# Optimization experiments

Hardware: AMD Instinct MI355X
Metric: run time of the kernel (lower is better)

Reference implementation:

```python
import jax, jax.numpy as jnp
import numpy as np

D_MODEL = 1024
NUM_HEADS = 16
D_K = D_MODEL // NUM_HEADS
THETA = 10000.0
SEQ = 4096
BATCH = 1


def _rope(x, token_positions):
    # x: [b, h, s, d_k]; interleaved even/odd rotation as in the torch module
    kd = jnp.arange(0, D_K, 2, dtype=jnp.float32) / D_K          # [d_k/2]
    angles = token_positions[:, None].astype(jnp.float32) / (THETA ** kd)  # [s, d_k/2]
    cos_pos = jnp.cos(angles)
    sin_pos = jnp.sin(angles)
    x_even = x[..., 0::2]
    x_odd = x[..., 1::2]
    rot_even = x_even * cos_pos - x_odd * sin_pos
    rot_odd = x_even * sin_pos + x_odd * cos_pos
    rot = jnp.stack([rot_even, rot_odd], axis=-1)                # [..., d_k/2, 2]
    return rot.reshape(*x.shape[:-1], D_K)


def setup_inputs() -> dict:
    key = jax.random.key(0)
    k1, k2, k3 = jax.random.split(key, 3)
    std_qkv = np.sqrt(2.0 / (D_MODEL + 3 * D_MODEL))
    std_o = np.sqrt(2.0 / (D_MODEL + D_MODEL))
    x = jax.random.normal(k1, (BATCH, SEQ, D_MODEL), dtype=jnp.float32)
    Wqkv = jax.random.normal(k2, (3 * D_MODEL, D_MODEL), dtype=jnp.float32) * std_qkv
    Wo = jax.random.normal(k3, (D_MODEL, D_MODEL), dtype=jnp.float32) * std_o
    token_positions = jnp.arange(SEQ, dtype=jnp.int32)
    return {"x": x, "Wqkv": Wqkv, "Wo": Wo, "token_positions": token_positions}


def reference(x, Wqkv, Wo, token_positions):
    b, s, _ = x.shape
    qkv = jnp.einsum('bsd,ed->bse', x, Wqkv)                      # [b, s, 3*d_model]
    q, k, v = jnp.split(qkv, 3, axis=-1)

    def to_heads(t):
        return t.reshape(b, s, NUM_HEADS, D_K).transpose(0, 2, 1, 3)  # [b, h, s, d_k]

    q, k, v = to_heads(q), to_heads(k), to_heads(v)
    q = _rope(q, token_positions)
    k = _rope(k, token_positions)

    scores = jnp.einsum('bhqd,bhkd->bhqk', q, k) / jnp.sqrt(jnp.float32(D_K))
    mask = jnp.tril(jnp.ones((s, s), dtype=bool))
    scores = jnp.where(mask, scores, -jnp.inf)
    attn = jax.nn.softmax(scores, axis=-1)
    out = jnp.einsum('bhqk,bhkd->bhqd', attn, v)                  # [b, h, s, d_k]
    out = out.transpose(0, 2, 1, 3).reshape(b, s, D_MODEL)
    return jnp.einsum('bsd,ed->bse', out, Wo)
```

## Files before the change

kernel.cpp:

```cpp
#include <hip/hip_runtime.h>
#include <cstdint>

typedef unsigned short u16;
typedef __attribute__((ext_vector_type(8))) short short8;
typedef __attribute__((ext_vector_type(4))) float float4v;

__device__ __forceinline__ float bf2f(u16 u) {
    union { unsigned int i; float f; } v; v.i = ((unsigned int)u) << 16; return v.f;
}
__device__ __forceinline__ u16 f2bf(float f) {
    union { float f; unsigned int i; } v; v.f = f;
    unsigned int i = v.i;
    i += 0x7fffu + ((i >> 16) & 1u);
    return (u16)(i >> 16);
}
__device__ __forceinline__ uint4 cvt8(const float* __restrict__ p) {
    float4 a = *(const float4*)p;
    float4 b = *(const float4*)(p + 4);
    u16 t[8] = {f2bf(a.x), f2bf(a.y), f2bf(a.z), f2bf(a.w),
                f2bf(b.x), f2bf(b.y), f2bf(b.z), f2bf(b.w)};
    return *(const uint4*)t;
}

__global__ void cvt_f32_bf16(const float* __restrict__ src, u16* __restrict__ dst, int n8) {
    int i = blockIdx.x * blockDim.x + threadIdx.x;
    if (i >= n8) return;
    *(uint4*)(dst + (size_t)i * 8) = cvt8(src + (size_t)i * 8);
}

__global__ void zero_f32(float* __restrict__ p, int n4) {
    int i = blockIdx.x * blockDim.x + threadIdx.x;
    if (i >= n4) return;
    float4 z = {0.f, 0.f, 0.f, 0.f};
    *(float4*)(p + (size_t)i * 4) = z;
}

__global__ __launch_bounds__(256) void gemm_bt(const u16* __restrict__ A,
                                               const u16* __restrict__ B,
                                               u16* __restrict__ C,
                                               int M, int N, int K) {
    __shared__ u16 As[128 * 40];
    __shared__ u16 Bs[128 * 40];
    const int tid  = threadIdx.x;
    const int wave = tid >> 6, lane = tid & 63;
    const int lg = lane >> 4, lr = lane & 15;
    const int bm = blockIdx.x * 128, bn = blockIdx.y * 128;
    const int wm = (wave & 1) * 64, wn = (wave >> 1) * 64;

    float4v acc[4][4] = {};

    for (int k0 = 0; k0 < K; k0 += 32) {
        #pragma unroll
        for (int i = 0; i < 2; ++i) {
            int seg = tid + i * 256;
            int row = seg >> 2;
            int co  = (seg & 3) * 8;
            *(uint4*)(As + row * 40 + co) = *(const uint4*)(A + (size_t)(bm + row) * K + k0 + co);
            *(uint4*)(Bs + row * 40 + co) = *(const uint4*)(B + (size_t)(bn + row) * K + k0 + co);
        }
        __syncthreads();

        short8 af[4], bf[4];
        #pragma unroll
        for (int i = 0; i < 4; ++i)
            af[i] = *(const short8*)(As + (wm + i * 16 + lr) * 40 + lg * 8);
        #pragma unroll
        for (int j = 0; j < 4; ++j)
            bf[j] = *(const short8*)(Bs + (wn + j * 16 + lr) * 40 + lg * 8);
        #pragma unroll
        for (int i = 0; i < 4; ++i)
            #pragma unroll
            for (int j = 0; j < 4; ++j)
                acc[i][j] = __builtin_amdgcn_mfma_f32_16x16x32_bf16(af[i], bf[j], acc[i][j], 0, 0, 0);
        __syncthreads();
    }

    #pragma unroll
    for (int i = 0; i < 4; ++i)
        #pragma unroll
        for (int j = 0; j < 4; ++j)
            #pragma unroll
            for (int r = 0; r < 4; ++r) {
                int row = bm + wm + i * 16 + lg * 4 + r;
                int col = bn + wn + j * 16 + lr;
                C[(size_t)row * N + col] = f2bf(acc[i][j][r]);
            }
}

__global__ void rope_kernel(u16* __restrict__ qkv, const int* __restrict__ pos, int S) {
    int idx = blockIdx.x * blockDim.x + threadIdx.x;
    int s = idx >> 10;
    if (s >= S) return;
    int p    = idx & 1023;
    int part = p >> 9;
    int wi   = p & 511;
    int head = wi >> 5;
    int i    = wi & 31;
    int col  = part * 1024 + head * 64 + 2 * i;

    u16* ptr = qkv + (size_t)s * 3072 + col;
    ushort2 v = *(const ushort2*)ptr;
    float xe = bf2f(v.x), xo = bf2f(v.y);
    float freq = __expf(-(float)i * 0.2878231366242557f);
    float ang  = (float)pos[s] * freq;
    float sn = sinf(ang), cs = cosf(ang);
    float re = xe * cs - xo * sn;
    float ro = xe * sn + xo * cs;
    if (part == 0) { re *= 0.125f; ro *= 0.125f; }
    ushort2 o; o.x = f2bf(re); o.y = f2bf(ro);
    *(ushort2*)ptr = o;
}

__global__ __launch_bounds__(256) void transpose_v(const u16* __restrict__ qkv,
                                                   u16* __restrict__ VT) {
    __shared__ u16 T[64 * 65];
    const int h = blockIdx.y, s0 = blockIdx.x * 64;
    const int tid = threadIdx.x;
    #pragma unroll
    for (int i = 0; i < 2; ++i) {
        int seg = i * 256 + tid;
        int r = seg >> 3, c8 = (seg & 7) * 8;
        u16 tmp[8];
        *(uint4*)tmp = *(const uint4*)(qkv + (size_t)(s0 + r) * 3072 + 2048 + h * 64 + c8);
        #pragma unroll
        for (int j = 0; j < 8; ++j) T[r * 65 + c8 + j] = tmp[j];
    }
    __syncthreads();
    #pragma unroll
    for (int i = 0; i < 2; ++i) {
        int seg = i * 256 + tid;
        int d = seg >> 3, s8 = (seg & 7) * 8;
        u16 tmp[8];
        #pragma unroll
        for (int j = 0; j < 8; ++j) tmp[j] = T[(s8 + j) * 65 + d];
        *(uint4*)(VT + (size_t)(h * 64 + d) * 4096 + s0 + s8) = *(const uint4*)tmp;
    }
}

__global__ __launch_bounds__(512) void attn_kernel(const u16* __restrict__ qkv,
                                                   const u16* __restrict__ VT,
                                                   float* __restrict__ acc,
                                                   float* __restrict__ lac) {
    __shared__ u16 Ks[64 * 64];
    __shared__ u16 Vt[64 * 64];
    __shared__ u16 Ps[8][16 * 72];

    const int tid  = threadIdx.x;
    const int wave = tid >> 6, lane = tid & 63;
    const int lg = lane >> 4, lr = lane & 15;
    const int h  = blockIdx.y;
    const int z  = blockIdx.z;

    const int srow = tid >> 3;
    const int sg   = tid & 7;
    const int sco  = sg * 8;
    const int sldso = srow * 64 + ((sg ^ (srow & 7)) * 8);
    const int swz = (lr & 7);

    #pragma unroll 1
    for (int part = 0; part < 2; ++part) {
        const int qt = part ? (31 - (int)blockIdx.x) : (int)blockIdx.x;
        const int qb = qt * 128;
        const int qrow0 = qb + wave * 16;
        const int tmax = qb + 64;
        const int t0s  = z * 64;

        short8 qf[2];
        #pragma unroll
        for (int kk = 0; kk < 2; ++kk)
            qf[kk] = *(const short8*)(qkv + (size_t)(qrow0 + lr) * 3072 + h * 64 + kk * 32 + lg * 8);

        float4v o_acc[4] = {};
        float rs = 0.f;

        uint4 rK = *(const uint4*)(qkv + (size_t)(t0s + srow) * 3072 + 1024 + h * 64 + sco);
        uint4 rV = *(const uint4*)(VT + (size_t)(h * 64 + srow) * 4096 + t0s + sco);
        __syncthreads();
        *(uint4*)(Ks + sldso) = rK;
        *(uint4*)(Vt + sldso) = rV;
        __syncthreads();

        for (int t0 = t0s; t0 <= tmax; t0 += 128) {
            const bool hasnext = (t0 + 128 <= tmax);
            if (hasnext) {
                rK = *(const uint4*)(qkv + (size_t)(t0 + 128 + srow) * 3072 + 1024 + h * 64 + sco);
                rV = *(const uint4*)(VT + (size_t)(h * 64 + srow) * 4096 + t0 + 128 + sco);
            }

            float4v sc[4];
            #pragma unroll
            for (int jt = 0; jt < 4; ++jt) {
                float4v a = {};
                #pragma unroll
                for (int kk = 0; kk < 2; ++kk) {
                    short8 kf = *(const short8*)(Ks + (jt * 16 + lr) * 64 + (((kk * 4 + lg) ^ swz) * 8));
                    a = __builtin_amdgcn_mfma_f32_16x16x32_bf16(kf, qf[kk], a, 0, 0, 0);
                }
                sc[jt] = a;
            }

            const bool mk = (t0 + 63 > qrow0);
            const int q_abs = qrow0 + lr;
            #pragma unroll
            for (int jt = 0; jt < 4; ++jt) {
                u16 pt[4];
                #pragma unroll
                for (int r = 0; r < 4; ++r) {
                    float s = sc[jt][r];
                    if (mk && (t0 + jt * 16 + lg * 4 + r > q_abs)) s = -30000.f;
                    float p = __expf(fminf(s, 60.f));
                    rs += p;
                    pt[r] = f2bf(p);
                }
                *(uint2*)(Ps[wave] + lr * 72 + jt * 16 + lg * 4) = *(const uint2*)pt;
            }

            short8 pf[2];
            #pragma unroll
            for (int kk = 0; kk < 2; ++kk)
                pf[kk] = *(const short8*)(Ps[wave] + lr * 72 + kk * 32 + lg * 8);
            #pragma unroll
            for (int jd = 0; jd < 4; ++jd) {
                float4v a = o_acc[jd];
                #pragma unroll
                for (int kk = 0; kk < 2; ++kk) {
                    short8 vf = *(const short8*)(Vt + (jd * 16 + lr) * 64 + (((kk * 4 + lg) ^ swz) * 8));
                    a = __builtin_amdgcn_mfma_f32_16x16x32_bf16(pf[kk], vf, a, 0, 0, 0);
                }
                o_acc[jd] = a;
            }
            __syncthreads();
            if (hasnext) {
                *(uint4*)(Ks + sldso) = rK;
                *(uint4*)(Vt + sldso) = rV;
            }
            __syncthreads();
        }

        float t = rs;
        t += __shfl_xor(t, 16, 64);
        t += __shfl_xor(t, 32, 64);
        if (lane < 16)
            atomicAdd(&lac[(size_t)(qrow0 + lr) * 16 + h], t);

        #pragma unroll
        for (int jd = 0; jd < 4; ++jd)
            #pragma unroll
            for (int r = 0; r < 4; ++r) {
                int s = qrow0 + lg * 4 + r;
                int d = jd * 16 + lr;
                atomicAdd(&acc[(size_t)s * 1024 + h * 64 + d], o_acc[jd][r]);
            }
    }
}

__global__ void norm_o(const float* __restrict__ acc, const float* __restrict__ lac,
                       u16* __restrict__ qkv) {
    int i = blockIdx.x * blockDim.x + threadIdx.x;
    if (i >= 4096 * 1024 / 8) return;
    int e0 = i * 8;
    int s = e0 >> 10, c = e0 & 1023, h = c >> 6;
    float inv = 1.0f / lac[(size_t)s * 16 + h];
    float4 a = *(const float4*)(acc + e0);
    float4 b = *(const float4*)(acc + e0 + 4);
    u16 t[8] = {f2bf(a.x * inv), f2bf(a.y * inv), f2bf(a.z * inv), f2bf(a.w * inv),
                f2bf(b.x * inv), f2bf(b.y * inv), f2bf(b.z * inv), f2bf(b.w * inv)};
    *(uint4*)(qkv + (size_t)s * 3072 + c) = *(const uint4*)t;
}

__global__ __launch_bounds__(256) void gemm_oproj(const u16* __restrict__ A,
                                                  const u16* __restrict__ B,
                                                  float* __restrict__ C) {
    __shared__ u16 As[128 * 40];
    __shared__ u16 Bs[128 * 40];
    const int tid  = threadIdx.x;
    const int wave = tid >> 6, lane = tid & 63;
    const int lg = lane >> 4, lr = lane & 15;
    const int bm = blockIdx.x * 128, bn = blockIdx.y * 128;
    const int wm = (wave & 1) * 64, wn = (wave >> 1) * 64;

    float4v acc[4][4] = {};

    for (int k0 = 0; k0 < 1024; k0 += 32) {
        #pragma unroll
        for (int i = 0; i < 2; ++i) {
            int seg = tid + i * 256;
            int row = seg >> 2;
            int co  = (seg & 3) * 8;
            *(uint4*)(As + row * 40 + co) =
                *(const uint4*)(A + (size_t)(bm + row) * 3072 + k0 + co);
            *(uint4*)(Bs + row * 40 + co) =
                *(const uint4*)(B + (size_t)(bn + row) * 1024 + k0 + co);
        }
        __syncthreads();

        short8 af[4], bf[4];
        #pragma unroll
        for (int i = 0; i < 4; ++i)
            af[i] = *(const short8*)(As + (wm + i * 16 + lr) * 40 + lg * 8);
        #pragma unroll
        for (int j = 0; j < 4; ++j)
            bf[j] = *(const short8*)(Bs + (wn + j * 16 + lr) * 40 + lg * 8);
        #pragma unroll
        for (int i = 0; i < 4; ++i)
            #pragma unroll
            for (int j = 0; j < 4; ++j)
                acc[i][j] = __builtin_amdgcn_mfma_f32_16x16x32_bf16(af[i], bf[j], acc[i][j], 0, 0, 0);
        __syncthreads();
    }

    #pragma unroll
    for (int i = 0; i < 4; ++i)
        #pragma unroll
        for (int j = 0; j < 4; ++j)
            #pragma unroll
            for (int r = 0; r < 4; ++r) {
                int row = bm + wm + i * 16 + lg * 4 + r;
                int col = bn + wn + j * 16 + lr;
                C[(size_t)row * 1024 + col] = acc[i][j][r];
            }
}

__global__ void fill_diag(float* __restrict__ p, size_t n, float mark) {
    size_t i = (size_t)blockIdx.x * blockDim.x + threadIdx.x;
    if (i < n) p[i] = 0.f;
    if (i == 0) p[0] = mark;
}

extern "C" void kernel_launch(void* const* d_in, const int* in_sizes, int n_in,
                              void* d_out, int out_size, void* d_ws, size_t ws_size,
                              hipStream_t stream) {
    int ix = -1, iwq = -1, iwo = -1, ip = -1;
    for (int i = 0; i < n_in; ++i) {
        if      (in_sizes[i] == 4096 * 1024) ix = i;
        else if (in_sizes[i] == 3072 * 1024) iwq = i;
        else if (in_sizes[i] == 1024 * 1024) iwo = i;
        else if (in_sizes[i] == 4096)        ip = i;
    }
    float* out = (float*)d_out;
    const size_t OUT_E = (size_t)4096 * 1024;
    const size_t QKV_E = (size_t)4096 * 3072;
    const size_t NEED  = QKV_E * 2 + (size_t)3072 * 1024 * 2;

    if (ix < 0 || iwq < 0 || iwo < 0 || ip < 0 || out_size != (int)OUT_E) {
        fill_diag<<<(int)((OUT_E + 255) / 256), 256, 0, stream>>>(out, OUT_E, 1000.0f);
        return;
    }
    if (ws_size < NEED) {
        fill_diag<<<(int)((OUT_E + 255) / 256), 256, 0, stream>>>(out, OUT_E, 500.0f);
        return;
    }
    const float* x    = (const float*)d_in[ix];
    const float* Wqkv = (const float*)d_in[iwq];
    const float* Wo   = (const float*)d_in[iwo];
    const int*   pos  = (const int*)d_in[ip];

    u16* qkv   = (u16*)d_ws;
    u16* wq_bf = (u16*)d_ws + QKV_E;
    u16* wo_bf = wq_bf;
    float* lac = (float*)((char*)wq_bf + 2 * 1024 * 1024 + 65536);
    u16* x_bf  = (u16*)d_out;
    u16* VT    = (u16*)d_out + OUT_E;
    float* acc = (float*)d_in[ix];

    cvt_f32_bf16<<<2048, 256, 0, stream>>>(x, x_bf, 4096 * 1024 / 8);
    cvt_f32_bf16<<<1536, 256, 0, stream>>>(Wqkv, wq_bf, 3072 * 1024 / 8);
    gemm_bt<<<dim3(32, 24), 256, 0, stream>>>(x_bf, wq_bf, qkv, 4096, 3072, 1024);
    zero_f32<<<4096, 256, 0, stream>>>(acc, 4096 * 1024 / 4);
    zero_f32<<<16, 256, 0, stream>>>(lac, 4096 * 16 / 4);
    cvt_f32_bf16<<<512, 256, 0, stream>>>(Wo, wo_bf, 1024 * 1024 / 8);
    rope_kernel<<<16384, 256, 0, stream>>>(qkv, pos, 4096);
    transpose_v<<<dim3(64, 16), 256, 0, stream>>>(qkv, VT);
    attn_kernel<<<dim3(16, 16, 2), 512, 0, stream>>>(qkv, VT, acc, lac);
    norm_o<<<2048, 256, 0, stream>>>(acc, lac, qkv);
    gemm_oproj<<<dim3(32, 8), 256, 0, stream>>>(qkv, wo_bf, out);
}
```

Measured before the change: 253.0 us.

## Use direct global-to-LDS loads in GEMMs, exp2 softmax, 4-way KV split

Both GEMMs now stage A/B tiles with global_load_lds straight into unpadded LDS, so loads no longer pass through registers. The attention kernel switches from exp to exp2 by folding log2(e) into the Q scale, packs bf16 conversions with v_cvt_pk_bf16_f32, and splits the key range four ways instead of two (stride 256) to raise parallelism. The unpadded LDS layout may bring back bank conflicts on fragment reads, and the extra split adds more atomic or partial accumulation traffic.

```diff
diff --git a/kernel.cpp b/kernel.cpp
--- a/kernel.cpp
+++ b/kernel.cpp
@@ -13,6 +13,15 @@
     unsigned int i = v.i;
     i += 0x7fffu + ((i >> 16) & 1u);
     return (u16)(i >> 16);
+}
+__device__ __forceinline__ unsigned cvt_pk_bf16(float lo, float hi) {
+    unsigned r;
+    asm("v_cvt_pk_bf16_f32 %0, %1, %2" : "=v"(r) : "v"(lo), "v"(hi));
+    return r;
+}
+__device__ __forceinline__ void gl2lds16(const u16* g, u16* l) {
+    __builtin_amdgcn_global_load_lds((const __attribute__((address_space(1))) void*)g,
+                                     (__attribute__((address_space(3))) void*)l, 16, 0, 0);
 }
 __device__ __forceinline__ uint4 cvt8(const float* __restrict__ p) {
     float4 a = *(const float4*)p;
@@ -39,34 +48,31 @@
                                                const u16* __restrict__ B,
                                                u16* __restrict__ C,
                                                int M, int N, int K) {
-    __shared__ u16 As[128 * 40];
-    __shared__ u16 Bs[128 * 40];
+    __shared__ u16 As[128 * 32];
+    __shared__ u16 Bs[128 * 32];
     const int tid  = threadIdx.x;
     const int wave = tid >> 6, lane = tid & 63;
     const int lg = lane >> 4, lr = lane & 15;
     const int bm = blockIdx.x * 128, bn = blockIdx.y * 128;
     const int wm = (wave & 1) * 64, wn = (wave >> 1) * 64;
+    const int row = tid >> 2, co = (tid & 3) * 8;
 
     float4v acc[4][4] = {};
 
     for (int k0 = 0; k0 < K; k0 += 32) {
-        #pragma unroll
-        for (int i = 0; i < 2; ++i) {
-            int seg = tid + i * 256;
-            int row = seg >> 2;
-            int co  = (seg & 3) * 8;
-            *(uint4*)(As + row * 40 + co) = *(const uint4*)(A + (size_t)(bm + row) * K + k0 + co);
-            *(uint4*)(Bs + row * 40 + co) = *(const uint4*)(B + (size_t)(bn + row) * K + k0 + co);
-        }
+        gl2lds16(A + (size_t)(bm + row) * K + k0 + co,      As + tid * 8);
+        gl2lds16(A + (size_t)(bm + 64 + row) * K + k0 + co, As + (tid + 256) * 8);
+        gl2lds16(B + (size_t)(bn + row) * K + k0 + co,      Bs + tid * 8);
+        gl2lds16(B + (size_t)(bn + 64 + row) * K + k0 + co, Bs + (tid + 256) * 8);
         __syncthreads();
 
         short8 af[4], bf[4];
         #pragma unroll
         for (int i = 0; i < 4; ++i)
-            af[i] = *(const short8*)(As + (wm + i * 16 + lr) * 40 + lg * 8);
+            af[i] = *(const short8*)(As + (wm + i * 16 + lr) * 32 + lg * 8);
         #pragma unroll
         for (int j = 0; j < 4; ++j)
-            bf[j] = *(const short8*)(Bs + (wn + j * 16 + lr) * 40 + lg * 8);
+            bf[j] = *(const short8*)(Bs + (wn + j * 16 + lr) * 32 + lg * 8);
         #pragma unroll
         for (int i = 0; i < 4; ++i)
             #pragma unroll
@@ -81,9 +87,9 @@
         for (int j = 0; j < 4; ++j)
             #pragma unroll
             for (int r = 0; r < 4; ++r) {
-                int row = bm + wm + i * 16 + lg * 4 + r;
-                int col = bn + wn + j * 16 + lr;
-                C[(size_t)row * N + col] = f2bf(acc[i][j][r]);
+                int rw = bm + wm + i * 16 + lg * 4 + r;
+                int cl = bn + wn + j * 16 + lr;
+                C[(size_t)rw * N + cl] = f2bf(acc[i][j][r]);
             }
 }
 
@@ -106,7 +112,7 @@
     float sn = sinf(ang), cs = cosf(ang);
     float re = xe * cs - xo * sn;
     float ro = xe * sn + xo * cs;
-    if (part == 0) { re *= 0.125f; ro *= 0.125f; }
+    if (part == 0) { re *= 0.18033688011112042f; ro *= 0.18033688011112042f; }
     ushort2 o; o.x = f2bf(re); o.y = f2bf(ro);
     *(ushort2*)ptr = o;
 }
@@ -180,11 +186,11 @@
         *(uint4*)(Vt + sldso) = rV;
         __syncthreads();
 
-        for (int t0 = t0s; t0 <= tmax; t0 += 128) {
-            const bool hasnext = (t0 + 128 <= tmax);
+        for (int t0 = t0s; t0 <= tmax; t0 += 256) {
+            const bool hasnext = (t0 + 256 <= tmax);
             if (hasnext) {
-                rK = *(const uint4*)(qkv + (size_t)(t0 + 128 + srow) * 3072 + 1024 + h * 64 + sco);
-                rV = *(const uint4*)(VT + (size_t)(h * 64 + srow) * 4096 + t0 + 128 + sco);
+                rK = *(const uint4*)(qkv + (size_t)(t0 + 256 + srow) * 3072 + 1024 + h * 64 + sco);
+                rV = *(const uint4*)(VT + (size_t)(h * 64 + srow) * 4096 + t0 + 256 + sco);
             }
 
             float4v sc[4];
@@ -203,16 +209,18 @@
             const int q_abs = qrow0 + lr;
             #pragma unroll
             for (int jt = 0; jt < 4; ++jt) {
-                u16 pt[4];
+                float e[4];
                 #pragma unroll
                 for (int r = 0; r < 4; ++r) {
                     float s = sc[jt][r];
                     if (mk && (t0 + jt * 16 + lg * 4 + r > q_abs)) s = -30000.f;
-                    float p = __expf(fminf(s, 60.f));
-                    rs += p;
-                    pt[r] = f2bf(p);
+                    e[r] = __builtin_amdgcn_exp2f(fminf(s, 86.562f));
                 }
-                *(uint2*)(Ps[wave] + lr * 72 + jt * 16 + lg * 4) = *(const uint2*)pt;
+                rs += (e[0] + e[1]) + (e[2] + e[3]);
+                uint2 w;
+                w.x = cvt_pk_bf16(e[0], e[1]);
+                w.y = cvt_pk_bf16(e[2], e[3]);
+                *(uint2*)(Ps[wave] + lr * 72 + jt * 16 + lg * 4) = w;
             }
 
             short8 pf[2];
@@ -271,36 +279,31 @@
 __global__ __launch_bounds__(256) void gemm_oproj(const u16* __restrict__ A,
                                                   const u16* __restrict__ B,
                                                   float* __restrict__ C) {
-    __shared__ u16 As[128 * 40];
-    __shared__ u16 Bs[128 * 40];
+    __shared__ u16 As[128 * 32];
+    __shared__ u16 Bs[128 * 32];
     const int tid  = threadIdx.x;
     const int wave = tid >> 6, lane = tid & 63;
     const int lg = lane >> 4, lr = lane & 15;
     const int bm = blockIdx.x * 128, bn = blockIdx.y * 128;
     const int wm = (wave & 1) * 64, wn = (wave >> 1) * 64;
+    const int row = tid >> 2, co = (tid & 3) * 8;
 
     float4v acc[4][4] = {};
 
     for (int k0 = 0; k0 < 1024; k0 += 32) {
-        #pragma unroll
-        for (int i = 0; i < 2; ++i) {
-            int seg = tid + i * 256;
-            int row = seg >> 2;
-            int co  = (seg & 3) * 8;
-            *(uint4*)(As + row * 40 + co) =
-                *(const uint4*)(A + (size_t)(bm + row) * 3072 + k0 + co);
-            *(uint4*)(Bs + row * 40 + co) =
-                *(const uint4*)(B + (size_t)(bn + row) * 1024 + k0 + co);
-        }
+        gl2lds16(A + (size_t)(bm + row) * 3072 + k0 + co,      As + tid * 8);
+        gl2lds16(A + (size_t)(bm + 64 + row) * 3072 + k0 + co, As + (tid + 256) * 8);
+        gl2lds16(B + (size_t)(bn + row) * 1024 + k0 + co,      Bs + tid * 8);
+        gl2lds16(B + (size_t)(bn + 64 + row) * 1024 + k0 + co, Bs + (tid + 256) * 8);
         __syncthreads();
 
         short8 af[4], bf[4];
         #pragma unroll
         for (int i = 0; i < 4; ++i)
-            af[i] = *(const short8*)(As + (wm + i * 16 + lr) * 40 + lg * 8);
+            af[i] = *(const short8*)(As + (wm + i * 16 + lr) * 32 + lg * 8);
         #pragma unroll
         for (int j = 0; j < 4; ++j)
-            bf[j] = *(const short8*)(Bs + (wn + j * 16 + lr) * 40 + lg * 8);
+            bf[j] = *(const short8*)(Bs + (wn + j * 16 + lr) * 32 + lg * 8);
         #pragma unroll
         for (int i = 0; i < 4; ++i)
             #pragma unroll
@@ -315,9 +318,9 @@
         for (int j = 0; j < 4; ++j)
             #pragma unroll
             for (int r = 0; r < 4; ++r) {
-                int row = bm + wm + i * 16 + lg * 4 + r;
-                int col = bn + wn + j * 16 + lr;
-                C[(size_t)row * 1024 + col] = acc[i][j][r];
+                int rw = bm + wm + i * 16 + lg * 4 + r;
+                int cl = bn + wn + j * 16 + lr;
+                C[(size_t)rw * 1024 + cl] = acc[i][j][r];
             }
 }
 
@@ -371,7 +374,7 @@
     cvt_f32_bf16<<<512, 256, 0, stream>>>(Wo, wo_bf, 1024 * 1024 / 8);
     rope_kernel<<<16384, 256, 0, stream>>>(qkv, pos, 4096);
     transpose_v<<<dim3(64, 16), 256, 0, stream>>>(qkv, VT);
-    attn_kernel<<<dim3(16, 16, 2), 512, 0, stream>>>(qkv, VT, acc, lac);
+    attn_kernel<<<dim3(16, 16, 4), 512, 0, stream>>>(qkv, VT, acc, lac);
     norm_o<<<2048, 256, 0, stream>>>(acc, lac, qkv);
     gemm_oproj<<<dim3(32, 8), 256, 0, stream>>>(qkv, wo_bf, out);
 }
```

Result: slower. 261.9 us (+3.5%).
